# Kernel optimization log

Measured on AMD Instinct MI355X. Metric: run time of the kernel, lower is better.

## Reference

```python
import jax, jax.numpy as jnp
import numpy as np

N, C, H, W = 8, 256, 64, 64
NW = 8            # n_win (regions per side)
TOPK = 4
HEADS = 16
MLP = 4 * C
SCALE = C ** -0.5  # qk_dim = dim in BiLevelRoutingAttention


def _ln(x, g, b, eps=1e-6):
    mu = x.mean(-1, keepdims=True)
    var = ((x - mu) ** 2).mean(-1, keepdims=True)
    return (x - mu) * jax.lax.rsqrt(var + eps) * g + b


def setup_inputs() -> dict:
    key = jax.random.key(0)
    ks = jax.random.split(key, 8)
    f = lambda k, shp: jax.random.normal(k, shp, jnp.float32) * 0.02
    return {
        "x": jax.random.normal(ks[0], (N, C, H, W), jnp.float32),
        "norm1_g": jnp.ones((C,), jnp.float32), "norm1_b": jnp.zeros((C,), jnp.float32),
        "qkv_w": f(ks[1], (C, 3 * C)), "qkv_b": jnp.zeros((3 * C,), jnp.float32),
        "lepe_w": f(ks[2], (5, 5, 1, C)), "lepe_b": jnp.zeros((C,), jnp.float32),
        "gamma1": -jnp.ones((C,), jnp.float32), "gamma2": -jnp.ones((C,), jnp.float32),
        "norm2_g": jnp.ones((C,), jnp.float32), "norm2_b": jnp.zeros((C,), jnp.float32),
        "mlp_w1": f(ks[3], (C, MLP)), "mlp_b1": jnp.zeros((MLP,), jnp.float32),
        "mlp_w2": f(ks[4], (MLP, C)), "mlp_b2": jnp.zeros((C,), jnp.float32),
    }


def _bra(x, qkv_w, qkv_b, lepe_w, lepe_b):
    # BiLevelRoutingAttention: x is NHWC
    n, hh, ww, c = x.shape
    h, w = hh // NW, ww // NW
    P, hw = NW * NW, h * w
    qkv = x @ qkv_w + qkv_b                    # [n,H,W,3c]
    q, k, v = qkv[..., :c], qkv[..., c:2 * c], qkv[..., 2 * c:]

    def win(t):                                 # [n,H,W,d] -> [n,P,h,w,d]
        d = t.shape[-1]
        return t.reshape(n, NW, h, NW, w, d).transpose(0, 1, 3, 2, 4, 5).reshape(n, P, h, w, d)

    qw, kw, vw = win(q), win(k), win(v)
    q_pix = qw.reshape(n, P, hw, c)
    k_pix = kw.reshape(n, P, hw, c)
    v_pix = vw.reshape(n, P, hw, c)

    # region-level routing (q/k detached; routing weights unused since mul_weight='none')
    q_win = jax.lax.stop_gradient(qw.mean((2, 3)))   # [n,P,c]
    k_win = jax.lax.stop_gradient(kw.mean((2, 3)))
    logit = jnp.einsum('npc,nqc->npq', q_win * SCALE, k_win)
    _, idx = jax.lax.top_k(logit, TOPK)              # [n,P,TOPK]

    gather = jax.vmap(lambda t, i: t[i])             # over batch
    k_sel = gather(k_pix, idx)                       # [n,P,TOPK,hw,c]
    v_sel = gather(v_pix, idx)

    dh = c // HEADS
    # channel layout is (m c): split heads on last dim
    qh = q_pix.reshape(n, P, hw, HEADS, dh).transpose(0, 1, 3, 2, 4)                       # [n,P,m,hw,dh]
    kh = k_sel.reshape(n, P, TOPK, hw, HEADS, dh).transpose(0, 1, 4, 2, 3, 5).reshape(n, P, HEADS, TOPK * hw, dh)
    vh = v_sel.reshape(n, P, TOPK, hw, HEADS, dh).transpose(0, 1, 4, 2, 3, 5).reshape(n, P, HEADS, TOPK * hw, dh)

    attn = jax.nn.softmax(jnp.einsum('npmqd,npmkd->npmqk', qh * SCALE, kh), axis=-1)
    out = jnp.einsum('npmqk,npmkd->npmqd', attn, vh)                                       # [n,P,m,hw,dh]
    out = out.transpose(0, 1, 3, 2, 4).reshape(n, P, hw, c)
    out = out.reshape(n, NW, NW, h, w, c).transpose(0, 1, 3, 2, 4, 5).reshape(n, hh, ww, c)

    # lepe: 5x5 depthwise conv over full-image v (side_dwconv=5)
    lepe = jax.lax.conv_general_dilated(
        v, lepe_w, (1, 1), 'SAME',
        dimension_numbers=('NHWC', 'HWIO', 'NHWC'),
        feature_group_count=c) + lepe_b
    return out + lepe   # wo = Identity for param_attention='qkv'


def reference(x, norm1_g, norm1_b, qkv_w, qkv_b, lepe_w, lepe_b, gamma1, gamma2,
              norm2_g, norm2_b, mlp_w1, mlp_b1, mlp_w2, mlp_b2):
    xp = x.transpose(0, 2, 3, 1)  # NCHW -> NHWC
    xp = xp + gamma1 * _bra(_ln(xp, norm1_g, norm1_b), qkv_w, qkv_b, lepe_w, lepe_b)
    z = _ln(xp, norm2_g, norm2_b)
    m = jax.nn.gelu(z @ mlp_w1 + mlp_b1, approximate=False) @ mlp_w2 + mlp_b2
    xp = xp + gamma2 * m
    return xp.transpose(0, 3, 1, 2)  # NHWC -> NCHW
```

## Files before the change

kernel.cpp:

```cpp
#include <hip/hip_runtime.h>

typedef unsigned short u16;
typedef __bf16 bf16x8 __attribute__((ext_vector_type(8)));
typedef short s16x4 __attribute__((ext_vector_type(4)));
typedef float f32x4 __attribute__((ext_vector_type(4)));

#define SCALE_ATT 0.0625f

static __device__ __forceinline__ u16 f2b(float f) {
    __bf16 h = (__bf16)f;
    union { __bf16 b; u16 u; } v; v.b = h;
    return v.u;
}
static __device__ __forceinline__ float b2f(u16 h) {
    union { unsigned u; float f; } v; v.u = ((unsigned)h) << 16;
    return v.f;
}

#if defined(__has_builtin)
#if __has_builtin(__builtin_amdgcn_mfma_f32_16x16x16bf16_1k)
#define HAVE_MFMA16 1
#endif
#if __has_builtin(__builtin_amdgcn_exp2f)
#define EXP2(x) __builtin_amdgcn_exp2f(x)
#endif
#if __has_builtin(__builtin_amdgcn_rcpf)
#define RCP(x) __builtin_amdgcn_rcpf(x)
#endif
#if __has_builtin(__builtin_amdgcn_global_load_lds)
#define HAVE_GLOADLDS 1
#endif
#endif
#ifndef EXP2
#define EXP2(x) exp2f(x)
#endif
#ifndef RCP
#define RCP(x) (1.0f / (x))
#endif

static __device__ __forceinline__ f32x4 mfma16(s16x4 a, s16x4 b, f32x4 c) {
#ifdef HAVE_MFMA16
    return __builtin_amdgcn_mfma_f32_16x16x16bf16_1k(a, b, c, 0, 0, 0);
#else
    f32x4 d;
    asm volatile("v_mfma_f32_16x16x16_bf16 %0, %1, %2, %3\n\ts_nop 7\n\ts_nop 7"
                 : "=v"(d) : "v"(a), "v"(b), "v"(c));
    return d;
#endif
}

#ifdef HAVE_GLOADLDS
static __device__ __forceinline__ void gload16(const u16* g, u16* l) {
    __builtin_amdgcn_global_load_lds(
        (const __attribute__((address_space(1))) void*)g,
        (__attribute__((address_space(3))) void*)l, 16, 0, 0);
}
#endif

static __device__ __forceinline__ float gelu_fast(float v) {
    float v2 = v * v;
    float w = fmaf(v2, 0.044715f, 1.0f);
    float arg = v * w * 2.30211754f;
    float e = EXP2(arg);
    float r = RCP(e + 1.0f);
    return fmaf(-v, r, v);
}

__global__ void wtrans3_kernel(const float* __restrict__ qkv_w,
                               const float* __restrict__ w1,
                               const float* __restrict__ w2,
                               u16* __restrict__ wt_qkv,
                               u16* __restrict__ wt_m1,
                               u16* __restrict__ wt_m2) {
    int i = blockIdx.x * 256 + threadIdx.x;
    if (i < 196608) {
        int r = i / 768, c = i % 768;
        wt_qkv[(size_t)c * 256 + r] = f2b(qkv_w[i]);
    } else if (i < 458752) {
        int j = i - 196608;
        int r = j >> 10, c = j & 1023;
        wt_m1[(size_t)c * 256 + r] = f2b(w1[j]);
    } else if (i < 720896) {
        int j = i - 458752;
        int r = j >> 8, c = j & 255;
        wt_m2[(size_t)c * 1024 + r] = f2b(w2[j]);
    }
}

__global__ __launch_bounds__(256) void ln_xpose_kernel(
    const float* __restrict__ x, const float* __restrict__ g, const float* __restrict__ b,
    u16* __restrict__ xp, u16* __restrict__ ln1, float* __restrict__ pool_part) {
    __shared__ float xs[256][65];
    __shared__ float ps[4][64], ps2[4][64];
    __shared__ float mvmu[64], mvrs[64];
    int nb = blockIdx.x; int n = nb >> 6, y = nb & 63;
    int t = threadIdx.x;
    const float4* src = (const float4*)(x + ((size_t)(n * 256 + t) * 64 + y) * 64);
    for (int x4 = 0; x4 < 16; ++x4) {
        float4 v = src[x4];
        xs[t][x4 * 4 + 0] = v.x; xs[t][x4 * 4 + 1] = v.y;
        xs[t][x4 * 4 + 2] = v.z; xs[t][x4 * 4 + 3] = v.w;
    }
    __syncthreads();
    int part = t >> 6, l = t & 63;
    float s1 = 0.f, s2 = 0.f;
    for (int c = 0; c < 64; ++c) { float v = xs[part * 64 + c][l]; s1 += v; s2 += v * v; }
    ps[part][l] = s1; ps2[part][l] = s2;
    __syncthreads();
    if (t < 64) {
        float su = ps[0][t] + ps[1][t] + ps[2][t] + ps[3][t];
        float sq = ps2[0][t] + ps2[1][t] + ps2[2][t] + ps2[3][t];
        float mu = su * (1.f / 256.f);
        float var = sq * (1.f / 256.f) - mu * mu;
        mvmu[t] = mu; mvrs[t] = rsqrtf(var + 1e-6f);
    }
    __syncthreads();
    float gc = g[t], bc = b[t];
    size_t tokbase = (size_t)nb * 64;
    float pw = 0.f;
    for (int xx = 0; xx < 64; ++xx) {
        float raw = xs[t][xx];
        float val = (raw - mvmu[xx]) * mvrs[xx] * gc + bc;
        size_t tok = tokbase + xx;
        xp[tok * 256 + t] = f2b(raw);
        ln1[tok * 256 + t] = f2b(val);
        pw += val;
        if ((xx & 7) == 7) {
            pool_part[((size_t)nb * 8 + (xx >> 3)) * 256 + t] = pw;
            pw = 0.f;
        }
    }
}

__global__ void pool_reduce_kernel(const float* __restrict__ pool_part,
                                   float* __restrict__ pooled) {
    int nb = blockIdx.x; int n = nb >> 6, p = nb & 63;
    int wi = p >> 3, wj = p & 7;
    int t = threadIdx.x;
    float s = 0.f;
    for (int r = 0; r < 8; ++r)
        s += pool_part[((size_t)((n * 64 + wi * 8 + r) * 8 + wj)) * 256 + t];
    pooled[(size_t)nb * 256 + t] = s * (1.f / 64.f);
}

__global__ void qkwin_kernel(const float* __restrict__ pooled,
                             const float* __restrict__ qkv_w, const float* __restrict__ qkv_b,
                             float* __restrict__ qk_win) {
    __shared__ float pr[256];
    int nb = blockIdx.x; int t = threadIdx.x;
    pr[t] = pooled[(size_t)nb * 256 + t];
    __syncthreads();
    float aq = qkv_b[t], ak = qkv_b[256 + t];
    for (int k = 0; k < 256; ++k) {
        float pv = pr[k];
        aq += pv * qkv_w[(size_t)k * 768 + t];
        ak += pv * qkv_w[(size_t)k * 768 + 256 + t];
    }
    qk_win[(size_t)nb * 512 + t] = aq;
    qk_win[(size_t)nb * 512 + 256 + t] = ak;
}

__global__ void routing_kernel(const float* __restrict__ qk_win, int* __restrict__ idxp) {
    __shared__ float lg_[64];
    int nb = blockIdx.x; int n = nb >> 6;
    int t = threadIdx.x;
    const float* qw = qk_win + (size_t)nb * 512;
    const float* kw = qk_win + (size_t)(n * 64 + t) * 512 + 256;
    float s = 0.f;
    for (int c = 0; c < 256; ++c) s += qw[c] * kw[c];
    lg_[t] = s * SCALE_ATT;
    __syncthreads();
    if (t == 0) {
        for (int j = 0; j < 4; ++j) {
            float best = -INFINITY; int bi = 0;
            for (int q = 0; q < 64; ++q) if (lg_[q] > best) { best = lg_[q]; bi = q; }
            idxp[nb * 4 + j] = bi;
            lg_[bi] = -INFINITY;
        }
    }
}

template <int EPI>
__global__ __launch_bounds__(256) void gemm_kernel(
    const u16* __restrict__ A, const u16* __restrict__ Bt,
    const float* __restrict__ bias, u16* __restrict__ outb,
    int M, int Nn, int K,
    const u16* __restrict__ resid_in, const float* __restrict__ gamma,
    float* __restrict__ resid_out) {
    __shared__ u16 smem[16384];
    u16* As = smem;
    u16* Bs = smem + 8192;
    int t = threadIdx.x;
    int rowBase = blockIdx.x * 128, colBase = blockIdx.y * 128;
    int wid = t >> 6, lane = t & 63;
    int wr = (wid >> 1) * 64, wc = (wid & 1) * 64;
    int lr = lane & 15, g = lane >> 4;
    f32x4 acc[4][4] = {};

    int rA0 = wid * 32 + (lane >> 2);
    int rA1 = rA0 + 16;
    int cs0 = (lane & 3) ^ ((rA0 >> 1) & 3);
    int cs1 = (lane & 3) ^ ((rA1 >> 1) & 3);
    const u16* gA0 = A + (size_t)(rowBase + rA0) * K + cs0 * 8;
    const u16* gA1 = A + (size_t)(rowBase + rA1) * K + cs1 * 8;
    const u16* gB0 = Bt + (size_t)(colBase + rA0) * K + cs0 * 8;
    const u16* gB1 = Bt + (size_t)(colBase + rA1) * K + cs1 * 8;
    u16* lA0 = &As[(wid * 2 + 0) * 512];
    u16* lA1 = &As[(wid * 2 + 1) * 512];
    u16* lB0 = &Bs[(wid * 2 + 0) * 512];
    u16* lB1 = &Bs[(wid * 2 + 1) * 512];

    int cSwz = (g * 16) ^ (((lr >> 1) & 3) << 4);
    const int NT = K >> 5;

#ifdef HAVE_GLOADLDS
    gload16(gA0, lA0);
    gload16(gA1, lA1);
    gload16(gB0, lB0);
    gload16(gB1, lB1);
    int cur = 0;
    for (int tk = 0; tk < NT; ++tk) {
        if (tk + 1 < NT) {
            int koff = (tk + 1) << 5;
            int bo = (cur ^ 1) << 12;
            gload16(gA0 + koff, lA0 + bo);
            gload16(gA1 + koff, lA1 + bo);
            gload16(gB0 + koff, lB0 + bo);
            gload16(gB1 + koff, lB1 + bo);
            asm volatile("s_waitcnt vmcnt(4)" ::: "memory");
        } else {
            asm volatile("s_waitcnt vmcnt(0)" ::: "memory");
        }
        __builtin_amdgcn_s_barrier();
        asm volatile("" ::: "memory");
        const char* pAc = (const char*)As + (cur << 13);
        const char* pBc = (const char*)Bs + (cur << 13);
        bf16x8 af[4], bfr[4];
        #pragma unroll
        for (int m = 0; m < 4; ++m)
            af[m] = *(const bf16x8*)(pAc + (wr + m * 16 + lr) * 64 + cSwz);
        #pragma unroll
        for (int nn = 0; nn < 4; ++nn)
            bfr[nn] = *(const bf16x8*)(pBc + (wc + nn * 16 + lr) * 64 + cSwz);
        #pragma unroll
        for (int m = 0; m < 4; ++m)
            #pragma unroll
            for (int nn = 0; nn < 4; ++nn)
                acc[m][nn] = __builtin_amdgcn_mfma_f32_16x16x32_bf16(af[m], bfr[nn], acc[m][nn], 0, 0, 0);
        asm volatile("" ::: "memory");
        __builtin_amdgcn_s_barrier();
        cur ^= 1;
    }
#else
    const char* pAc = (const char*)As;
    const char* pBc = (const char*)Bs;
    for (int tk = 0; tk < NT; ++tk) {
        int koff = tk << 5;
        float4 a0 = *(const float4*)(gA0 + koff);
        float4 a1 = *(const float4*)(gA1 + koff);
        float4 b0 = *(const float4*)(gB0 + koff);
        float4 b1 = *(const float4*)(gB1 + koff);
        __syncthreads();
        *(float4*)&lA0[lane * 8] = a0;
        *(float4*)&lA1[lane * 8] = a1;
        *(float4*)&lB0[lane * 8] = b0;
        *(float4*)&lB1[lane * 8] = b1;
        __syncthreads();
        bf16x8 af[4], bfr[4];
        #pragma unroll
        for (int m = 0; m < 4; ++m)
            af[m] = *(const bf16x8*)(pAc + (wr + m * 16 + lr) * 64 + cSwz);
        #pragma unroll
        for (int nn = 0; nn < 4; ++nn)
            bfr[nn] = *(const bf16x8*)(pBc + (wc + nn * 16 + lr) * 64 + cSwz);
        #pragma unroll
        for (int m = 0; m < 4; ++m)
            #pragma unroll
            for (int nn = 0; nn < 4; ++nn)
                acc[m][nn] = __builtin_amdgcn_mfma_f32_16x16x32_bf16(af[m], bfr[nn], acc[m][nn], 0, 0, 0);
        __syncthreads();
    }
#endif
    if constexpr (EPI == 2) {
        int n = rowBase >> 12;
        int y0 = (rowBase >> 6) & 63;
        float* ts = (float*)smem;
        #pragma unroll
        for (int half = 0; half < 2; ++half) {
            if ((wid & 1) == half) {
                #pragma unroll
                for (int m = 0; m < 4; ++m)
                    #pragma unroll
                    for (int nn = 0; nn < 4; ++nn) {
                        int colL = nn * 16 + lr;
                        int col = colBase + half * 64 + colL;
                        float bcol = bias[col];
                        float gcol = gamma[col];
                        int s = ((colL & 7) << 2) | ((colL >> 3) & 1);
                        #pragma unroll
                        for (int r = 0; r < 4; ++r) {
                            int rowIdx = wr + m * 16 + g * 4 + r;
                            float v = acc[m][nn][r] + bcol;
                            float yv = b2f(resid_in[(size_t)(rowBase + rowIdx) * 256 + col]) + gcol * v;
                            ts[colL * 128 + (rowIdx ^ s)] = yv;
                        }
                    }
            }
            __syncthreads();
            #pragma unroll
            for (int j = 0; j < 16; ++j) {
                int ch = wid * 16 + j;
                int s = ((ch & 7) << 2) | ((ch >> 3) & 1);
                float v0 = ts[ch * 128 + (lane ^ s)];
                float v1 = ts[ch * 128 + ((64 + lane) ^ s)];
                float* gb = resid_out + ((size_t)(n * 256 + colBase + half * 64 + ch) * 64 + y0) * 64;
                gb[lane] = v0;
                gb[64 + lane] = v1;
            }
            __syncthreads();
        }
    } else {
        #pragma unroll
        for (int m = 0; m < 4; ++m)
            #pragma unroll
            for (int nn = 0; nn < 4; ++nn) {
                int col = colBase + wc + nn * 16 + lr;
                float bcol = bias[col];
                #pragma unroll
                for (int r = 0; r < 4; ++r) {
                    int row = rowBase + wr + m * 16 + g * 4 + r;
                    float v = acc[m][nn][r] + bcol;
                    if constexpr (EPI == 0) {
                        outb[(size_t)row * Nn + col] = f2b(v);
                    } else {
                        outb[(size_t)row * Nn + col] = f2b(gelu_fast(v));
                    }
                }
            }
    }
}

__global__ __launch_bounds__(512) void attn_lepe_kernel(
    const u16* __restrict__ qkv, const int* __restrict__ idxp,
    const float* __restrict__ lw, const float* __restrict__ lb,
    u16* __restrict__ attn_out, u16* __restrict__ lepe_out) {
    __shared__ __align__(16) char smem_[40960];
    int t = threadIdx.x;
    if (blockIdx.y >= 8) {
        u16 (*vt)[64][64] = (u16 (*)[64][64])smem_;
        int nb = blockIdx.x, cg = blockIdx.y - 8;
        int n = nb >> 6, y = nb & 63;
        {
            int xs = t >> 3, cs = t & 7;
            #pragma unroll
            for (int r = 0; r < 5; ++r) {
                int yy = y - 2 + r;
                bool ok = (yy >= 0 && yy <= 63);
                float4 v = {0.f, 0.f, 0.f, 0.f};
                if (ok)
                    v = *(const float4*)(qkv +
                        ((size_t)((n * 64 + yy) * 64 + xs)) * 768 + 512 + cg * 64 + cs * 8);
                *(float4*)&vt[r][xs][cs * 8] = v;
            }
        }
        __syncthreads();
        int c = t & 63, x0 = (t >> 6) * 8;
        float wv[25];
        #pragma unroll
        for (int i = 0; i < 25; ++i) wv[i] = lw[i * 256 + cg * 64 + c];
        float bc = lb[cg * 64 + c];
        float win[5][5];
        #pragma unroll
        for (int r = 0; r < 5; ++r)
            #pragma unroll
            for (int j = 0; j < 4; ++j) {
                int x2 = x0 - 2 + j;
                win[r][j] = (x2 >= 0) ? b2f(vt[r][x2][c]) : 0.f;
            }
        #pragma unroll
        for (int xi = 0; xi < 8; ++xi) {
            int xx = x0 + xi;
            int xl = xx + 2;
            #pragma unroll
            for (int r = 0; r < 5; ++r)
                win[r][4] = (xl <= 63) ? b2f(vt[r][xl][c]) : 0.f;
            float s = bc;
            #pragma unroll
            for (int r = 0; r < 5; ++r)
                #pragma unroll
                for (int j = 0; j < 5; ++j)
                    s = fmaf(wv[r * 5 + j], win[r][j], s);
            lepe_out[((size_t)nb * 64 + xx) * 256 + cg * 64 + c] = f2b(s);
            #pragma unroll
            for (int r = 0; r < 5; ++r)
                #pragma unroll
                for (int j = 0; j < 4; ++j)
                    win[r][j] = win[r][j + 1];
        }
        return;
    }
    u16 (*qs)[36]   = (u16 (*)[36])smem_;
    u16 (*ks)[36]   = (u16 (*)[36])(smem_ + 4608);
    u16 (*vts)[256] = (u16 (*)[256])(smem_ + 23040);
    float (*os)[36] = (float (*)[36])(smem_ + 4608);
    int nb = blockIdx.x, hg = blockIdx.y;
    int n = nb >> 6, p = nb & 63;
    int y0 = (p >> 3) * 8, x0 = (p & 7) * 8;
    int w0 = idxp[nb * 4 + 0], w1 = idxp[nb * 4 + 1];
    int w2 = idxp[nb * 4 + 2], w3 = idxp[nb * 4 + 3];
    {
        int tok = t >> 3, seg = t & 7;
        int tokg = (n * 64 + y0 + (tok >> 3)) * 64 + x0 + (tok & 7);
        *(uint2*)&qs[tok][seg * 4] =
            *(const uint2*)(qkv + (size_t)tokg * 768 + hg * 32 + seg * 4);
    }
    {
        int key = t & 255, half = t >> 8;
        int ws = (key >> 6) == 0 ? w0 : (key >> 6) == 1 ? w1 : (key >> 6) == 2 ? w2 : w3;
        int kp = key & 63;
        int tokk = (n * 64 + (ws >> 3) * 8 + (kp >> 3)) * 64 + (ws & 7) * 8 + (kp & 7);
        const u16* kbase = qkv + (size_t)tokk * 768 + 256 + hg * 32 + half * 16;
        *(uint2*)&ks[key][half * 16 + 0]  = *(const uint2*)(kbase + 0);
        *(uint2*)&ks[key][half * 16 + 4]  = *(const uint2*)(kbase + 4);
        *(uint2*)&ks[key][half * 16 + 8]  = *(const uint2*)(kbase + 8);
        *(uint2*)&ks[key][half * 16 + 12] = *(const uint2*)(kbase + 12);
        const u16* vbase = kbase + 256;
        union { float4 f[2]; u16 u[16]; } vu;
        vu.f[0] = *(const float4*)vbase;
        vu.f[1] = *(const float4*)(vbase + 8);
        #pragma unroll
        for (int c2 = 0; c2 < 16; ++c2)
            vts[half * 16 + c2][key ^ (c2 << 2)] = vu.u[c2];
    }
    __syncthreads();

    int wid = t >> 6, lane = t & 63, lr = lane & 15, g = lane >> 4;
    int hh = wid & 1, q0 = (wid >> 1) * 16, c0 = hh * 16;
    f32x4 zf4 = {0.f, 0.f, 0.f, 0.f};
    s16x4 qf = *(const s16x4*)&qs[q0 + lr][c0 + g * 4];
    f32x4 sacc[16];
    __builtin_amdgcn_s_setprio(1);
    #pragma unroll
    for (int kt = 0; kt < 16; ++kt) {
        s16x4 kf = *(const s16x4*)&ks[kt * 16 + lr][c0 + g * 4];
        sacc[kt] = mfma16(kf, qf, zf4);
    }
    __builtin_amdgcn_s_setprio(0);
    float mx = fmaxf(fmaxf(sacc[0][0], sacc[0][1]), fmaxf(sacc[0][2], sacc[0][3]));
    #pragma unroll
    for (int kt = 1; kt < 16; ++kt) {
        mx = fmaxf(mx, fmaxf(sacc[kt][0], sacc[kt][1]));
        mx = fmaxf(mx, fmaxf(sacc[kt][2], sacc[kt][3]));
    }
    mx = fmaxf(mx, __shfl_xor(mx, 16, 64));
    mx = fmaxf(mx, __shfl_xor(mx, 32, 64));
    const float k1 = 0.09016844005556021f;
    float negmk = -mx * k1;
    float dsum = 0.f;
    s16x4 pf[16];
    #pragma unroll
    for (int kt = 0; kt < 16; ++kt) {
        float e0 = EXP2(fmaf(sacc[kt][0], k1, negmk));
        float e1 = EXP2(fmaf(sacc[kt][1], k1, negmk));
        float e2 = EXP2(fmaf(sacc[kt][2], k1, negmk));
        float e3 = EXP2(fmaf(sacc[kt][3], k1, negmk));
        dsum += (e0 + e1) + (e2 + e3);
        union { unsigned u[2]; s16x4 s; } pk;
        asm("v_cvt_pk_bf16_f32 %0, %1, %2" : "=v"(pk.u[0]) : "v"(e0), "v"(e1));
        asm("v_cvt_pk_bf16_f32 %0, %1, %2" : "=v"(pk.u[1]) : "v"(e2), "v"(e3));
        pf[kt] = pk.s;
    }
    dsum += __shfl_xor(dsum, 16, 64);
    dsum += __shfl_xor(dsum, 32, 64);
    float rden = 1.f / dsum;
    __syncthreads();
    f32x4 o0 = zf4, o1 = zf4;
    __builtin_amdgcn_s_setprio(1);
    #pragma unroll
    for (int kt = 0; kt < 16; kt += 2) {
        s16x4 v0 = *(const s16x4*)&vts[c0 + lr][(kt * 16 + g * 4) ^ (lr << 2)];
        o0 = mfma16(v0, pf[kt], o0);
        s16x4 v1 = *(const s16x4*)&vts[c0 + lr][((kt + 1) * 16 + g * 4) ^ (lr << 2)];
        o1 = mfma16(v1, pf[kt + 1], o1);
    }
    __builtin_amdgcn_s_setprio(0);
    #pragma unroll
    for (int r = 0; r < 4; ++r)
        os[q0 + lr][c0 + g * 4 + r] = (o0[r] + o1[r]) * rden;
    __syncthreads();
    {
        int tok = t >> 3, cs = (t & 7) * 4;
        int tokg = (n * 64 + y0 + (tok >> 3)) * 64 + x0 + (tok & 7);
        float f0 = os[tok][cs + 0], f1 = os[tok][cs + 1];
        float f2 = os[tok][cs + 2], f3 = os[tok][cs + 3];
        uint2 pk;
        asm("v_cvt_pk_bf16_f32 %0, %1, %2" : "=v"(pk.x) : "v"(f0), "v"(f1));
        asm("v_cvt_pk_bf16_f32 %0, %1, %2" : "=v"(pk.y) : "v"(f2), "v"(f3));
        *(uint2*)(attn_out + (size_t)tokg * 256 + hg * 32 + cs) = pk;
    }
}

__global__ __launch_bounds__(256) void resid1_ln2_kernel(
    const u16* __restrict__ xp, const u16* __restrict__ attn,
    const u16* __restrict__ lepe, const float* __restrict__ g1,
    const float* __restrict__ n2g, const float* __restrict__ n2b,
    u16* __restrict__ xp1, u16* __restrict__ z) {
    int t = threadIdx.x;
    int wid = t >> 6, lane = t & 63;
    size_t tok = (size_t)blockIdx.x * 4 + wid;
    size_t base = tok * 256 + lane * 4;
    uint2 xv = *(const uint2*)(xp + base);
    uint2 av = *(const uint2*)(attn + base);
    uint2 lv = *(const uint2*)(lepe + base);
    float4 g1v = *(const float4*)(g1 + lane * 4);
    float4 ngv = *(const float4*)(n2g + lane * 4);
    float4 nbv = *(const float4*)(n2b + lane * 4);
    const u16* xu = (const u16*)&xv;
    const u16* au = (const u16*)&av;
    const u16* lu = (const u16*)&lv;
    const float* g1f = (const float*)&g1v;
    const float* ngf = (const float*)&ngv;
    const float* nbf = (const float*)&nbv;
    float x1[4];
    float s1 = 0.f, s2 = 0.f;
    #pragma unroll
    for (int j = 0; j < 4; ++j) {
        float xx = b2f(xu[j]) + g1f[j] * (b2f(au[j]) + b2f(lu[j]));
        x1[j] = xx; s1 += xx; s2 += xx * xx;
    }
    #pragma unroll
    for (int off = 1; off < 64; off <<= 1) {
        s1 += __shfl_xor(s1, off, 64);
        s2 += __shfl_xor(s2, off, 64);
    }
    float mu = s1 * (1.f / 256.f);
    float var = s2 * (1.f / 256.f) - mu * mu;
    float rs = rsqrtf(var + 1e-6f);
    u16 zo[4], xo[4];
    #pragma unroll
    for (int j = 0; j < 4; ++j) {
        zo[j] = f2b((x1[j] - mu) * rs * ngf[j] + nbf[j]);
        xo[j] = f2b(x1[j]);
    }
    *(uint2*)(z + base) = *(uint2*)zo;
    *(uint2*)(xp1 + base) = *(uint2*)xo;
}

extern "C" void kernel_launch(void* const* d_in, const int* in_sizes, int n_in,
                              void* d_out, int out_size, void* d_ws, size_t ws_size,
                              hipStream_t stream) {
    (void)in_sizes; (void)n_in; (void)out_size; (void)ws_size;
    const float* x      = (const float*)d_in[0];
    const float* n1g    = (const float*)d_in[1];
    const float* n1b    = (const float*)d_in[2];
    const float* qkv_w  = (const float*)d_in[3];
    const float* qkv_b  = (const float*)d_in[4];
    const float* lepe_w = (const float*)d_in[5];
    const float* lepe_b = (const float*)d_in[6];
    const float* g1     = (const float*)d_in[7];
    const float* g2     = (const float*)d_in[8];
    const float* n2g    = (const float*)d_in[9];
    const float* n2b    = (const float*)d_in[10];
    const float* w1     = (const float*)d_in[11];
    const float* b1     = (const float*)d_in[12];
    const float* w2     = (const float*)d_in[13];
    const float* b2     = (const float*)d_in[14];
    float* outp = (float*)d_out;
    char* ws = (char*)d_ws;

    u16*   xp_b      = (u16*)(ws + 0);
    u16*   ln1       = (u16*)(ws + 33554432);
    u16*   qkv       = (u16*)(ws + 50331648);
    u16*   attn_b    = (u16*)(ws + 100663296);
    u16*   lepe      = (u16*)(ws + 134217728);
    u16*   zbuf      = (u16*)(ws + 150994944);
    float* pool_part = (float*)(ws + 167772160);
    float* pooled    = (float*)(ws + 171966464);
    float* qk_win    = (float*)(ws + 172490752);
    int*   idxb      = (int*)(ws + 173539328);
    u16*   wt_qkv    = (u16*)(ws + 173547520);
    u16*   wt_m1     = (u16*)(ws + 173940736);
    u16*   wt_m2     = (u16*)(ws + 174465024);
    u16*   hbuf      = ln1;

    wtrans3_kernel<<<2816, 256, 0, stream>>>(qkv_w, w1, w2, wt_qkv, wt_m1, wt_m2);

    ln_xpose_kernel<<<512, 256, 0, stream>>>(x, n1g, n1b, xp_b, ln1, pool_part);
    pool_reduce_kernel<<<512, 256, 0, stream>>>(pool_part, pooled);
    qkwin_kernel<<<512, 256, 0, stream>>>(pooled, qkv_w, qkv_b, qk_win);
    routing_kernel<<<512, 64, 0, stream>>>(qk_win, idxb);

    gemm_kernel<0><<<dim3(256, 6), 256, 0, stream>>>(
        ln1, wt_qkv, qkv_b, qkv, 32768, 768, 256, nullptr, nullptr, nullptr);

    attn_lepe_kernel<<<dim3(512, 12), 512, 0, stream>>>(
        qkv, idxb, lepe_w, lepe_b, attn_b, lepe);

    resid1_ln2_kernel<<<8192, 256, 0, stream>>>(xp_b, attn_b, lepe, g1, n2g, n2b, xp_b, zbuf);

    gemm_kernel<1><<<dim3(256, 8), 256, 0, stream>>>(
        zbuf, wt_m1, b1, hbuf, 32768, 1024, 256, nullptr, nullptr, nullptr);
    gemm_kernel<2><<<dim3(256, 2), 256, 0, stream>>>(
        hbuf, wt_m2, b2, nullptr, 32768, 256, 1024, xp_b, g2, outp);
}
```

Measured before the change: 227.7 us.

## Deepen GEMM LDS pipeline to four stages, two k-tiles per barrier

The GEMM main loop moves from a double-buffered LDS ring with one 32-wide k-tile per iteration to a four-slot ring that prefetches two k-tiles ahead and computes two k-tiles between barriers. This halves the number of barriers per K and keeps more global loads in flight to hide memory latency. In exchange, shared memory per block doubles to 64 KB, which may cut the number of resident blocks per CU. The loop also assumes NT is even.

```diff
diff --git a/kernel.cpp b/kernel.cpp
--- a/kernel.cpp
+++ b/kernel.cpp
@@ -187,9 +187,9 @@
     int M, int Nn, int K,
     const u16* __restrict__ resid_in, const float* __restrict__ gamma,
     float* __restrict__ resid_out) {
-    __shared__ u16 smem[16384];
+    __shared__ u16 smem[32768];
     u16* As = smem;
-    u16* Bs = smem + 8192;
+    u16* Bs = smem + 16384;
     int t = threadIdx.x;
     int rowBase = blockIdx.x * 128, colBase = blockIdx.y * 128;
     int wid = t >> 6, lane = t & 63;
@@ -214,42 +214,43 @@
     const int NT = K >> 5;
 
 #ifdef HAVE_GLOADLDS
-    gload16(gA0, lA0);
-    gload16(gA1, lA1);
-    gload16(gB0, lB0);
-    gload16(gB1, lB1);
-    int cur = 0;
-    for (int tk = 0; tk < NT; ++tk) {
-        if (tk + 1 < NT) {
-            int koff = (tk + 1) << 5;
-            int bo = (cur ^ 1) << 12;
-            gload16(gA0 + koff, lA0 + bo);
-            gload16(gA1 + koff, lA1 + bo);
-            gload16(gB0 + koff, lB0 + bo);
-            gload16(gB1 + koff, lB1 + bo);
-            asm volatile("s_waitcnt vmcnt(4)" ::: "memory");
+    gload16(gA0, lA0);            gload16(gA1, lA1);
+    gload16(gB0, lB0);            gload16(gB1, lB1);
+    gload16(gA0 + 32, lA0 + 4096); gload16(gA1 + 32, lA1 + 4096);
+    gload16(gB0 + 32, lB0 + 4096); gload16(gB1 + 32, lB1 + 4096);
+    for (int tk = 0; tk < NT; tk += 2) {
+        if (tk + 2 < NT) {
+            int k2 = (tk + 2) << 5, k3 = (tk + 3) << 5;
+            int b2 = ((tk + 2) & 3) * 4096, b3 = ((tk + 3) & 3) * 4096;
+            gload16(gA0 + k2, lA0 + b2); gload16(gA1 + k2, lA1 + b2);
+            gload16(gB0 + k2, lB0 + b2); gload16(gB1 + k2, lB1 + b2);
+            gload16(gA0 + k3, lA0 + b3); gload16(gA1 + k3, lA1 + b3);
+            gload16(gB0 + k3, lB0 + b3); gload16(gB1 + k3, lB1 + b3);
+            asm volatile("s_waitcnt vmcnt(8)" ::: "memory");
         } else {
             asm volatile("s_waitcnt vmcnt(0)" ::: "memory");
         }
         __builtin_amdgcn_s_barrier();
         asm volatile("" ::: "memory");
-        const char* pAc = (const char*)As + (cur << 13);
-        const char* pBc = (const char*)Bs + (cur << 13);
-        bf16x8 af[4], bfr[4];
-        #pragma unroll
-        for (int m = 0; m < 4; ++m)
-            af[m] = *(const bf16x8*)(pAc + (wr + m * 16 + lr) * 64 + cSwz);
-        #pragma unroll
-        for (int nn = 0; nn < 4; ++nn)
-            bfr[nn] = *(const bf16x8*)(pBc + (wc + nn * 16 + lr) * 64 + cSwz);
-        #pragma unroll
-        for (int m = 0; m < 4; ++m)
+        #pragma unroll
+        for (int s = 0; s < 2; ++s) {
+            const char* pAc = (const char*)As + (((tk + s) & 3) << 13);
+            const char* pBc = (const char*)Bs + (((tk + s) & 3) << 13);
+            bf16x8 af[4], bfr[4];
+            #pragma unroll
+            for (int m = 0; m < 4; ++m)
+                af[m] = *(const bf16x8*)(pAc + (wr + m * 16 + lr) * 64 + cSwz);
             #pragma unroll
             for (int nn = 0; nn < 4; ++nn)
-                acc[m][nn] = __builtin_amdgcn_mfma_f32_16x16x32_bf16(af[m], bfr[nn], acc[m][nn], 0, 0, 0);
+                bfr[nn] = *(const bf16x8*)(pBc + (wc + nn * 16 + lr) * 64 + cSwz);
+            #pragma unroll
+            for (int m = 0; m < 4; ++m)
+                #pragma unroll
+                for (int nn = 0; nn < 4; ++nn)
+                    acc[m][nn] = __builtin_amdgcn_mfma_f32_16x16x32_bf16(af[m], bfr[nn], acc[m][nn], 0, 0, 0);
+        }
         asm volatile("" ::: "memory");
         __builtin_amdgcn_s_barrier();
-        cur ^= 1;
     }
 #else
     const char* pAc = (const char*)As;
```

Measured after the change: 228.5 us. About the same (+0.4%).
